# Optimization experiments

Measured on AMD Instinct MI355X. Metric: run time of the kernel, lower is better.

## Reference

```python
import jax, jax.numpy as jnp
import numpy as np

L = 4       # num_layers
H = 64      # hidden
EPS_BN = 1e-5


def _edge_mlp_bn(e, W1, b1, W2, b2, g, bt):
    # Sequential(Linear, ReLU, Linear, ReLU, BatchNorm1d) in training mode
    h = jax.nn.relu(e @ W1 + b1)
    h = jax.nn.relu(h @ W2 + b2)
    mu = jnp.mean(h, axis=0)
    var = jnp.mean((h - mu) ** 2, axis=0)  # biased variance (torch BN train)
    return (h - mu) * jax.lax.rsqrt(var + EPS_BN) * g + bt


def _bip_layer(src, tgt, ei, eattr, p, i):
    # p = (eW1, eb1, eW2, eb2, g, bt, lW, lb, rW), each stacked over layers
    eW1, eb1, eW2, eb2, g, bt, lW, lb, rW = (q[i] for q in p)
    emb = _edge_mlp_bn(eattr, eW1, eb1, eW2, eb2, g, bt)
    msg = jax.nn.relu(src[ei[0]] + emb)                         # [E, H]
    n_t = tgt.shape[0]
    agg = jax.ops.segment_sum(msg, ei[1], num_segments=n_t)
    cnt = jax.ops.segment_sum(jnp.ones((ei.shape[1],), msg.dtype), ei[1],
                              num_segments=n_t)
    out = agg / jnp.maximum(cnt, 1.0)[:, None]                  # mean aggr
    out = out @ lW + lb + tgt @ rW                              # lin_l + lin_r
    nrm = jnp.linalg.norm(out, axis=-1, keepdims=True)
    return out / jnp.maximum(nrm, 1e-12)                        # F.normalize


def setup_inputs() -> dict:
    key = jax.random.key(0)
    ks = iter(jax.random.split(key, 64))
    Nv = Nc = 100000
    Ev = Ec = 1250000
    d = {}
    d["var_node_features"] = jax.random.normal(next(ks), (Nv, 2), jnp.float32)
    d["con_node_features"] = jax.random.normal(next(ks), (Nc, 2), jnp.float32)
    d["edge_features_var"] = jax.random.normal(next(ks), (Ev, 1), jnp.float32)
    d["edge_features_con"] = jax.random.normal(next(ks), (Ec, 1), jnp.float32)
    d["edge_index_var"] = jax.random.randint(next(ks), (2, Ev), 0, Nv, jnp.int32)
    d["edge_index_con"] = jax.random.randint(next(ks), (2, Ec), 0, Nc, jnp.int32)

    def lin(k, shape, fan_in):
        return jax.random.normal(k, shape, jnp.float32) * (2.0 / fan_in) ** 0.5

    # node encoders: Linear(2,H), ReLU, Linear(H,H)
    for nm in ("enc_v", "enc_c"):
        d[nm + "_W1"] = lin(next(ks), (2, H), 2)
        d[nm + "_b1"] = jnp.zeros((H,), jnp.float32)
        d[nm + "_W2"] = lin(next(ks), (H, H), H)
        d[nm + "_b2"] = jnp.zeros((H,), jnp.float32)

    # bipartite layers (lv_* = layers_var, lc_* = layers_con), stacked over L
    for nm in ("lv", "lc"):
        d[nm + "_eW1"] = lin(next(ks), (L, 1, H), 1)
        d[nm + "_eb1"] = jnp.zeros((L, H), jnp.float32)
        d[nm + "_eW2"] = lin(next(ks), (L, H, H), H)
        d[nm + "_eb2"] = jnp.zeros((L, H), jnp.float32)
        d[nm + "_g"] = jnp.ones((L, H), jnp.float32)
        d[nm + "_bt"] = jnp.zeros((L, H), jnp.float32)
        d[nm + "_lW"] = lin(next(ks), (L, H, H), H)
        d[nm + "_lb"] = jnp.zeros((L, H), jnp.float32)
        d[nm + "_rW"] = lin(next(ks), (L, H, H), H)

    d["lin1_W"] = lin(next(ks), ((L + 1) * H, H), (L + 1) * H)
    d["lin1_b"] = jnp.zeros((H,), jnp.float32)
    d["lin2_W"] = lin(next(ks), (H, H), H)
    d["lin2_b"] = jnp.zeros((H,), jnp.float32)
    d["lin3_W"] = lin(next(ks), (H, H), H)
    d["lin3_b"] = jnp.zeros((H,), jnp.float32)
    d["lin4_W"] = lin(next(ks), (H, 2), H)
    d["lin4_b"] = jnp.zeros((2,), jnp.float32)
    return d


def reference(var_node_features, con_node_features, edge_features_var,
              edge_features_con, edge_index_var, edge_index_con,
              enc_v_W1, enc_v_b1, enc_v_W2, enc_v_b2,
              enc_c_W1, enc_c_b1, enc_c_W2, enc_c_b2,
              lv_eW1, lv_eb1, lv_eW2, lv_eb2, lv_g, lv_bt, lv_lW, lv_lb, lv_rW,
              lc_eW1, lc_eb1, lc_eW2, lc_eb2, lc_g, lc_bt, lc_lW, lc_lb, lc_rW,
              lin1_W, lin1_b, lin2_W, lin2_b, lin3_W, lin3_b, lin4_W, lin4_b):
    xv = jax.nn.relu(var_node_features @ enc_v_W1 + enc_v_b1) @ enc_v_W2 + enc_v_b2
    xc = jax.nn.relu(con_node_features @ enc_c_W1 + enc_c_b1) @ enc_c_W2 + enc_c_b2
    lvp = (lv_eW1, lv_eb1, lv_eW2, lv_eb2, lv_g, lv_bt, lv_lW, lv_lb, lv_rW)
    lcp = (lc_eW1, lc_eb1, lc_eW2, lc_eb2, lc_g, lc_bt, lc_lW, lc_lb, lc_rW)
    x_var = [xv]
    for i in range(L):
        # var -> con pass (layers_var), then con -> var pass (layers_con)
        xc = jax.nn.relu(_bip_layer(xv, xc, edge_index_var, edge_features_var, lvp, i))
        xv = jax.nn.relu(_bip_layer(xc, xv, edge_index_con, edge_features_con, lcp, i))
        x_var.append(xv)
    x = jnp.concatenate(x_var, axis=-1)                         # [Nv, (L+1)H]
    x = jax.nn.relu(x @ lin1_W + lin1_b)
    x = jax.nn.relu(x @ lin2_W + lin2_b)
    x = jax.nn.relu(x @ lin3_W + lin3_b)
    x = x @ lin4_W + lin4_b
    return jax.nn.log_softmax(x, axis=-1)
```

## Files before the change

### kernel.cpp

```cpp
#include <hip/hip_runtime.h>
#include <math.h>

__device__ __forceinline__ float readlane_f(float v, int l) {
    return __int_as_float(__builtin_amdgcn_readlane(__float_as_int(v), l));
}
__device__ __forceinline__ unsigned readlane_u(unsigned v, int l) {
    return (unsigned)__builtin_amdgcn_readlane((int)v, l);
}

__global__ __launch_bounds__(256) void enc_kernel(
    const float* __restrict__ feat, const float* __restrict__ W1,
    const float* __restrict__ b1, const float* __restrict__ W2,
    const float* __restrict__ b2, float* __restrict__ out, int N)
{
    __shared__ float sW2[64 * 64];
    __shared__ float sh1[64 * 64];
    const int n0 = blockIdx.x * 64;
    const int t = threadIdx.x;
    for (int idx = t; idx < 4096; idx += 256) sW2[idx] = W2[idx];
    for (int idx = t; idx < 4096; idx += 256) {
        int n = idx >> 6, j = idx & 63;
        int gn = n0 + n;
        float v = 0.f;
        if (gn < N) {
            float f0 = feat[gn * 2 + 0], f1 = feat[gn * 2 + 1];
            v = fmaxf(fmaf(f0, W1[j], fmaf(f1, W1[64 + j], b1[j])), 0.f);
        }
        sh1[idx] = v;
    }
    __syncthreads();
    for (int idx = t; idx < 4096; idx += 256) {
        int n = idx >> 6, k = idx & 63;
        int gn = n0 + n;
        if (gn >= N) continue;
        float acc = b2[k];
        const float* hrow = &sh1[n * 64];
        #pragma unroll 8
        for (int j = 0; j < 64; ++j) acc = fmaf(hrow[j], sW2[j * 64 + k], acc);
        out[gn * 64 + k] = acc;
    }
}

__global__ __launch_bounds__(256) void build_tables_all_kernel(
    const float* __restrict__ lv_eW1, const float* __restrict__ lv_eb1,
    const float* __restrict__ lv_eW2, const float* __restrict__ lv_eb2,
    const float* __restrict__ lc_eW1, const float* __restrict__ lc_eb1,
    const float* __restrict__ lc_eW2, const float* __restrict__ lc_eb2,
    float* __restrict__ PQ8, float* __restrict__ sortedT8)
{
    const int cfg = blockIdx.x;
    const int li = (cfg < 4) ? cfg : cfg - 4;
    const float* eW1 = ((cfg < 4) ? lv_eW1 : lc_eW1) + li * 64;
    const float* eb1 = ((cfg < 4) ? lv_eb1 : lc_eb1) + li * 64;
    const float* eW2 = ((cfg < 4) ? lv_eW2 : lc_eW2) + li * 4096;
    const float* eb2 = ((cfg < 4) ? lv_eb2 : lc_eb2) + li * 64;
    float* PQ = PQ8 + cfg * 65 * 128;
    float* sortedT = sortedT8 + cfg * 64;

    __shared__ float sa[64], sb[64], sT[64];
    __shared__ int srank[64];
    const int t = threadIdx.x;
    if (t < 64) {
        float a = eW1[t], b = eb1[t];
        sa[t] = a; sb[t] = b;
        sT[t] = (a != 0.f) ? (-b / a) : INFINITY;
    }
    __syncthreads();
    if (t < 64) {
        float Tj = sT[t];
        int r = 0;
        for (int i = 0; i < 64; ++i) {
            float Ti = sT[i];
            r += (Ti < Tj || (Ti == Tj && i < t)) ? 1 : 0;
        }
        srank[t] = r;
        sortedT[r] = Tj;
    }
    __syncthreads();
    for (int idx = t; idx < 65 * 64; idx += 256) {
        int iv = idx >> 6, k = idx & 63;
        float accP = 0.f, accQ = 0.f;
        for (int j = 0; j < 64; ++j) {
            float a = sa[j];
            bool act = (a > 0.f) ? (srank[j] < iv)
                                 : ((a < 0.f) ? (srank[j] >= iv) : (sb[j] > 0.f));
            if (act) {
                float w = eW2[j * 64 + k];
                accP = fmaf(a, w, accP);
                accQ = fmaf(sb[j], w, accQ);
            }
        }
        PQ[idx * 2 + 0] = accP;
        PQ[idx * 2 + 1] = accQ + eb2[k];
    }
}

__device__ __forceinline__ int interval_of(const float* sT, float ev)
{
    int iv = 0;
    #pragma unroll
    for (int s = 32; s >= 1; s >>= 1)
        if (iv + s <= 64 && sT[iv + s - 1] < ev) iv += s;
    return iv;
}

__global__ __launch_bounds__(256) void edge_stats_all_kernel(
    const float* __restrict__ efv, const float* __restrict__ efc, int Ev, int Ec,
    const float* __restrict__ PQ8, const float* __restrict__ sortedT8,
    double* __restrict__ stage, int NSB)
{
    const int cfg = blockIdx.y;
    const float* ef = (cfg < 4) ? efv : efc;
    const int E = (cfg < 4) ? Ev : Ec;
    const float2* __restrict__ PQg = (const float2*)(PQ8 + cfg * 65 * 128);
    const float* sortedT = sortedT8 + cfg * 64;

    __shared__ float sT[64];
    __shared__ double sred[2][4][64];
    const int t = threadIdx.x;
    if (t < 64) sT[t] = sortedT[t];
    __syncthreads();
    const int lane = t & 63, wave = t >> 6;
    const int gw = blockIdx.x * 4 + wave;
    const int nW = NSB * 4;
    double sum = 0.0, sq = 0.0;
    const int nTiles = (E + 63) >> 6;
    for (int tile = gw; tile < nTiles; tile += nW) {
        const int p = tile << 6;
        const int m = min(64, E - p);
        float ev = 0.f; int iv = 0;
        if (lane < m) {
            ev = ef[p + lane];
            iv = interval_of(sT, ev);
        }
        for (int c = 0; c < m; c += 16) {
            if (c + 16 <= m) {
                float h[16];
                #pragma unroll
                for (int k = 0; k < 16; ++k) {
                    float sev = readlane_f(ev, c + k);
                    int siv = __builtin_amdgcn_readlane(iv, c + k);
                    float2 pq = PQg[siv * 64 + lane];
                    h[k] = fmaxf(fmaf(sev, pq.x, pq.y), 0.f);
                }
                #pragma unroll
                for (int k = 0; k < 16; ++k) {
                    sum += (double)h[k];
                    sq = fma((double)h[k], (double)h[k], sq);
                }
            } else {
                for (int k = c; k < m; ++k) {
                    float sev = readlane_f(ev, k);
                    int siv = __builtin_amdgcn_readlane(iv, k);
                    float2 pq = PQg[siv * 64 + lane];
                    float h = fmaxf(fmaf(sev, pq.x, pq.y), 0.f);
                    sum += (double)h;
                    sq = fma((double)h, (double)h, sq);
                }
            }
        }
    }
    sred[0][wave][lane] = sum;
    sred[1][wave][lane] = sq;
    __syncthreads();
    if (t < 128) {
        int s = t >> 6, k = t & 63;
        double v = sred[s][0][k] + sred[s][1][k] + sred[s][2][k] + sred[s][3][k];
        stage[((size_t)(cfg * NSB + blockIdx.x) * 2 + s) * 64 + k] = v;
    }
}

__global__ __launch_bounds__(128) void bn_finalize_all_kernel(
    const double* __restrict__ stage, int NSB,
    const float* __restrict__ lv_g, const float* __restrict__ lv_bt,
    const float* __restrict__ lc_g, const float* __restrict__ lc_bt,
    int Ev, int Ec, float* __restrict__ stv)
{
    const int cfg = blockIdx.x;
    const int t = threadIdx.x;
    const int s = t >> 6, k = t & 63;
    double a = 0.0;
    for (int b = 0; b < NSB; ++b)
        a += stage[((size_t)(cfg * NSB + b) * 2 + s) * 64 + k];
    __shared__ double sh[2][64];
    sh[s][k] = a;
    __syncthreads();
    if (t < 64) {
        double En = (double)((cfg < 4) ? Ev : Ec);
        double mu = sh[0][k] / En;
        double var = sh[1][k] / En - mu * mu;
        if (var < 0.0) var = 0.0;
        const int li = (cfg < 4) ? cfg : cfg - 4;
        const float* g  = ((cfg < 4) ? lv_g  : lc_g)  + li * 64;
        const float* bt = ((cfg < 4) ? lv_bt : lc_bt) + li * 64;
        double sc = (double)g[k] / sqrt(var + 1e-5);
        stv[cfg * 128 + k] = (float)sc;
        stv[cfg * 128 + 64 + k] = (float)((double)bt[k] - mu * sc);
    }
}

__global__ void count_kernel(const int* __restrict__ tgt_idx,
                             int* __restrict__ cnt, int E)
{
    int i = blockIdx.x * blockDim.x + threadIdx.x;
    if (i < E) atomicAdd(&cnt[tgt_idx[i]], 1);
}

__global__ __launch_bounds__(256) void scan1_kernel(const int* __restrict__ cnt,
                                                    int* __restrict__ bsum, int N)
{
    __shared__ int sred[256];
    const int b = blockIdx.x, t = threadIdx.x;
    const int base = b * 1024;
    int s = 0;
    for (int i = t; i < 1024; i += 256) {
        int g = base + i;
        s += (g < N) ? cnt[g] : 0;
    }
    sred[t] = s; __syncthreads();
    for (int o = 128; o > 0; o >>= 1) {
        if (t < o) sred[t] += sred[t + o];
        __syncthreads();
    }
    if (t == 0) bsum[b] = sred[0];
}

__global__ __launch_bounds__(1024) void scan2_kernel(int* __restrict__ bsum, int G,
                                                     int* __restrict__ rowptr_last, int E)
{
    __shared__ int s[1024];
    const int t = threadIdx.x;
    int v = (t < G) ? bsum[t] : 0;
    s[t] = v; __syncthreads();
    for (int o = 1; o < 1024; o <<= 1) {
        int x = (t >= o) ? s[t - o] : 0;
        __syncthreads();
        s[t] += x;
        __syncthreads();
    }
    if (t < G) bsum[t] = s[t] - v;
    if (t == 0) *rowptr_last = E;
}

__global__ __launch_bounds__(256) void scan3_kernel(const int* __restrict__ cnt,
                                                    const int* __restrict__ bsum,
                                                    int* __restrict__ rowptr,
                                                    int* __restrict__ cursor, int N)
{
    __shared__ int sthr[256];
    const int b = blockIdx.x, t = threadIdx.x;
    const int base = b * 1024 + t * 4;
    int loc[4]; int run = 0;
    #pragma unroll
    for (int j = 0; j < 4; ++j) {
        int g = base + j;
        int c = (g < N) ? cnt[g] : 0;
        loc[j] = run; run += c;
    }
    sthr[t] = run; __syncthreads();
    int own = run;
    for (int o = 1; o < 256; o <<= 1) {
        int x = (t >= o) ? sthr[t - o] : 0;
        __syncthreads();
        sthr[t] += x;
        __syncthreads();
    }
    int ex = sthr[t] - own + bsum[b];
    #pragma unroll
    for (int j = 0; j < 4; ++j) {
        int g = base + j;
        if (g < N) { rowptr[g] = ex + loc[j]; cursor[g] = ex + loc[j]; }
    }
}

__global__ void scatter_kernel(const float* __restrict__ ef, const int* __restrict__ ei,
                               int* __restrict__ cursor, float* __restrict__ efp,
                               int* __restrict__ srcp, int E)
{
    int e = blockIdx.x * blockDim.x + threadIdx.x;
    if (e < E) {
        int tg = ei[E + e];
        int pos = atomicAdd(&cursor[tg], 1);
        efp[pos] = ef[e];
        srcp[pos] = ei[e];
    }
}

template <bool FUSE_ACC>
__global__ __launch_bounds__(256) void layer_kernel(
    const float* __restrict__ efp, const int* __restrict__ srcp,
    const int* __restrict__ rowptr, const float* __restrict__ src,
    float* __restrict__ tgt,
    const float* __restrict__ PQ, const float* __restrict__ sortedT,
    const float* __restrict__ st,
    const float* __restrict__ lW, const float* __restrict__ lb,
    const float* __restrict__ rW,
    const float* __restrict__ accW, float* __restrict__ acc, int N)
{
    __shared__ float sU[4096];
    __shared__ float sAgg[64][65];
    __shared__ float sT[64];
    __shared__ int   sRp[65];
    __shared__ float part[4][64];
    __shared__ float srn[64];

    const int t = threadIdx.x, lane = t & 63, wave = t >> 6;
    const int n0 = blockIdx.x * 64;
    const float2* __restrict__ PQg = (const float2*)PQ;

    for (int i = t; i < 64 * 65; i += 256) (&sAgg[0][0])[i] = 0.f;
    if (t < 64) sT[t] = sortedT[t];
    if (t < 65) sRp[t] = rowptr[min(n0 + t, N)];
    __syncthreads();

    const float ssv = st[lane], ttv = st[64 + lane];
    const int e0 = sRp[0], e1 = sRp[64];
    float racc = 0.f;
    for (int tb = e0 + wave * 64; tb < e1; tb += 256) {
        const int m = min(64, e1 - tb);
        float ev = 0.f; unsigned pk = 0; bool bndb = false;
        if (lane < m) {
            int g = tb + lane;
            ev = efp[g];
            unsigned is = (unsigned)srcp[g];
            int lo = 0;
            #pragma unroll
            for (int s = 32; s >= 1; s >>= 1) {
                int c = lo + s;
                if (c <= 63 && sRp[c] <= g) lo = c;
            }
            bndb = (g + 1 == sRp[lo + 1]);
            unsigned iv = (unsigned)interval_of(sT, ev);
            pk = is | (iv << 18) | ((unsigned)lo << 25) | (bndb ? (1u << 31) : 0u);
        }
        const unsigned long long bm = __ballot(bndb);
        for (int c = 0; c < m; c += 16) {
            if (c + 16 <= m) {
                float msg[16];
                #pragma unroll
                for (int k = 0; k < 16; ++k) {
                    float sev = readlane_f(ev, c + k);
                    unsigned spk = readlane_u(pk, c + k);
                    float2 pq = PQg[((spk >> 18) & 0x7Fu) * 64 + lane];
                    float h = fmaxf(fmaf(sev, pq.x, pq.y), 0.f);
                    msg[k] = fmaxf(src[(size_t)(spk & 0x3FFFFu) * 64 + lane]
                                   + fmaf(h, ssv, ttv), 0.f);
                }
                #pragma unroll
                for (int k = 0; k < 16; ++k) {
                    racc += msg[k];
                    if ((bm >> (c + k)) & 1ull) {
                        unsigned spk = readlane_u(pk, c + k);
                        int l = (int)((spk >> 25) & 63u);
                        float inv = 1.f / (float)(sRp[l + 1] - sRp[l]);
                        atomicAdd(&sAgg[l][lane], racc * inv);
                        racc = 0.f;
                    }
                }
            } else {
                for (int k = c; k < m; ++k) {
                    float sev = readlane_f(ev, k);
                    unsigned spk = readlane_u(pk, k);
                    float2 pq = PQg[((spk >> 18) & 0x7Fu) * 64 + lane];
                    float h = fmaxf(fmaf(sev, pq.x, pq.y), 0.f);
                    float msg = fmaxf(src[(size_t)(spk & 0x3FFFFu) * 64 + lane]
                                      + fmaf(h, ssv, ttv), 0.f);
                    racc += msg;
                    if ((bm >> k) & 1ull) {
                        int l = (int)((spk >> 25) & 63u);
                        float inv = 1.f / (float)(sRp[l + 1] - sRp[l]);
                        atomicAdd(&sAgg[l][lane], racc * inv);
                        racc = 0.f;
                    }
                }
            }
        }
        if (racc != 0.f) {
            unsigned spk = readlane_u(pk, m - 1);
            int l = (int)((spk >> 25) & 63u);
            float inv = 1.f / (float)(sRp[l + 1] - sRp[l]);
            atomicAdd(&sAgg[l][lane], racc * inv);
            racc = 0.f;
        }
    }
    __syncthreads();

    for (int idx = t; idx < 4096; idx += 256) sU[idx] = lW[idx];
    __syncthreads();
    const int n = lane;
    float o[16];
    {
        const float* mr = sAgg[n];
        for (int m4 = 0; m4 < 4; ++m4) {
            const int kb = (wave + m4 * 4) * 4;
            float o0 = 0, o1 = 0, o2 = 0, o3 = 0;
            #pragma unroll 8
            for (int j = 0; j < 64; ++j) {
                float mv = mr[j];
                float4 w4 = *reinterpret_cast<const float4*>(&sU[j * 64 + kb]);
                o0 = fmaf(mv, w4.x, o0); o1 = fmaf(mv, w4.y, o1);
                o2 = fmaf(mv, w4.z, o2); o3 = fmaf(mv, w4.w, o3);
            }
            o[m4 * 4 + 0] = o0; o[m4 * 4 + 1] = o1;
            o[m4 * 4 + 2] = o2; o[m4 * 4 + 3] = o3;
        }
    }
    __syncthreads();
    for (int idx = t; idx < 4096; idx += 256) sU[idx] = rW[idx];
    for (int idx = t; idx < 4096; idx += 256) {
        int nn = idx >> 6, j = idx & 63;
        int gn = n0 + nn;
        sAgg[nn][j] = (gn < N) ? tgt[(size_t)gn * 64 + j] : 0.f;
    }
    __syncthreads();
    float ssq = 0.f;
    {
        const float* tr = sAgg[n];
        for (int m4 = 0; m4 < 4; ++m4) {
            const int kb = (wave + m4 * 4) * 4;
            float o0 = o[m4 * 4 + 0], o1 = o[m4 * 4 + 1];
            float o2 = o[m4 * 4 + 2], o3 = o[m4 * 4 + 3];
            #pragma unroll 8
            for (int j = 0; j < 64; ++j) {
                float tv = tr[j];
                float4 w4 = *reinterpret_cast<const float4*>(&sU[j * 64 + kb]);
                o0 = fmaf(tv, w4.x, o0); o1 = fmaf(tv, w4.y, o1);
                o2 = fmaf(tv, w4.z, o2); o3 = fmaf(tv, w4.w, o3);
            }
            o0 += lb[kb + 0]; o1 += lb[kb + 1]; o2 += lb[kb + 2]; o3 += lb[kb + 3];
            o[m4 * 4 + 0] = o0; o[m4 * 4 + 1] = o1;
            o[m4 * 4 + 2] = o2; o[m4 * 4 + 3] = o3;
            ssq = fmaf(o0, o0, fmaf(o1, o1, fmaf(o2, o2, fmaf(o3, o3, ssq))));
        }
    }
    part[wave][n] = ssq;
    __syncthreads();
    if (t < 64) {
        float s = part[0][t] + part[1][t] + part[2][t] + part[3][t];
        srn[t] = 1.f / fmaxf(sqrtf(s), 1e-12f);
    }
    for (int m4 = 0; m4 < 4; ++m4) {
        const int kb = (wave + m4 * 4) * 4;
        sAgg[n][kb + 0] = o[m4 * 4 + 0];
        sAgg[n][kb + 1] = o[m4 * 4 + 1];
        sAgg[n][kb + 2] = o[m4 * 4 + 2];
        sAgg[n][kb + 3] = o[m4 * 4 + 3];
    }
    __syncthreads();
    for (int idx = t; idx < 4096; idx += 256) {
        int nn = idx >> 6, k = idx & 63;
        int gn = n0 + nn;
        float v = fmaxf((&sAgg[0][0])[nn * 65 + k] * srn[nn], 0.f);
        if (gn < N) tgt[(size_t)gn * 64 + k] = v;
        if (FUSE_ACC) (&sAgg[0][0])[nn * 65 + k] = v;
    }
    if (FUSE_ACC) {
        __syncthreads();
        for (int idx = t; idx < 4096; idx += 256) sU[idx] = accW[idx];
        __syncthreads();
        const float* xr = sAgg[n];
        const int gn = n0 + n;
        for (int m4 = 0; m4 < 4; ++m4) {
            const int kb = (wave + m4 * 4) * 4;
            float o0 = 0, o1 = 0, o2 = 0, o3 = 0;
            #pragma unroll 8
            for (int j = 0; j < 64; ++j) {
                float xv = xr[j];
                float4 w4 = *reinterpret_cast<const float4*>(&sU[j * 64 + kb]);
                o0 = fmaf(xv, w4.x, o0); o1 = fmaf(xv, w4.y, o1);
                o2 = fmaf(xv, w4.z, o2); o3 = fmaf(xv, w4.w, o3);
            }
            if (gn < N) {
                float4* ap = reinterpret_cast<float4*>(&acc[(size_t)gn * 64 + kb]);
                float4 old = *ap;
                *ap = make_float4(old.x + o0, old.y + o1, old.z + o2, old.w + o3);
            }
        }
    }
}

__global__ __launch_bounds__(256) void acc_gemm_init_kernel(
    const float* __restrict__ X, const float* __restrict__ W,
    float* __restrict__ acc, int N)
{
    __shared__ float sW[64 * 64];
    __shared__ float sX[64][65];
    const int n0 = blockIdx.x * 64;
    const int t = threadIdx.x;
    for (int idx = t; idx < 4096; idx += 256) sW[idx] = W[idx];
    for (int idx = t; idx < 4096; idx += 256) {
        int n = idx >> 6, j = idx & 63;
        int gn = n0 + n;
        sX[n][j] = (gn < N) ? X[gn * 64 + j] : 0.f;
    }
    __syncthreads();
    const int n = t & 63;
    const int gn = n0 + n;
    for (int m4 = 0; m4 < 4; ++m4) {
        int kb = ((t >> 6) + m4 * 4) * 4;
        float o0 = 0, o1 = 0, o2 = 0, o3 = 0;
        const float* xr = sX[n];
        #pragma unroll 8
        for (int j = 0; j < 64; ++j) {
            float xv = xr[j];
            float4 w4 = *reinterpret_cast<const float4*>(&sW[j * 64 + kb]);
            o0 = fmaf(xv, w4.x, o0); o1 = fmaf(xv, w4.y, o1);
            o2 = fmaf(xv, w4.z, o2); o3 = fmaf(xv, w4.w, o3);
        }
        if (gn < N)
            *reinterpret_cast<float4*>(&acc[(size_t)gn * 64 + kb]) =
                make_float4(o0, o1, o2, o3);
    }
}

__global__ __launch_bounds__(256) void final_kernel(
    const float* __restrict__ acc, const float* __restrict__ b1,
    const float* __restrict__ W2, const float* __restrict__ b2,
    const float* __restrict__ W3, const float* __restrict__ b3,
    const float* __restrict__ W4, const float* __restrict__ b4,
    float* __restrict__ out, int N)
{
    __shared__ float sW[64 * 64];
    __shared__ float sA[64][65], sB[64][65];
    __shared__ float sy[64][2];
    const int n0 = blockIdx.x * 64;
    const int t = threadIdx.x;
    for (int idx = t; idx < 4096; idx += 256) sW[idx] = W2[idx];
    for (int idx = t; idx < 4096; idx += 256) {
        int n = idx >> 6, j = idx & 63;
        int gn = n0 + n;
        sA[n][j] = (gn < N) ? fmaxf(acc[gn * 64 + j] + b1[j], 0.f) : 0.f;
    }
    __syncthreads();
    const int n = t & 63;
    for (int m4 = 0; m4 < 4; ++m4) {
        int kb = ((t >> 6) + m4 * 4) * 4;
        float o0 = 0, o1 = 0, o2 = 0, o3 = 0;
        const float* xr = sA[n];
        #pragma unroll 8
        for (int j = 0; j < 64; ++j) {
            float xv = xr[j];
            float4 w4 = *reinterpret_cast<const float4*>(&sW[j * 64 + kb]);
            o0 = fmaf(xv, w4.x, o0); o1 = fmaf(xv, w4.y, o1);
            o2 = fmaf(xv, w4.z, o2); o3 = fmaf(xv, w4.w, o3);
        }
        sB[n][kb + 0] = fmaxf(o0 + b2[kb + 0], 0.f);
        sB[n][kb + 1] = fmaxf(o1 + b2[kb + 1], 0.f);
        sB[n][kb + 2] = fmaxf(o2 + b2[kb + 2], 0.f);
        sB[n][kb + 3] = fmaxf(o3 + b2[kb + 3], 0.f);
    }
    __syncthreads();
    for (int idx = t; idx < 4096; idx += 256) sW[idx] = W3[idx];
    __syncthreads();
    for (int m4 = 0; m4 < 4; ++m4) {
        int kb = ((t >> 6) + m4 * 4) * 4;
        float o0 = 0, o1 = 0, o2 = 0, o3 = 0;
        const float* xr = sB[n];
        #pragma unroll 8
        for (int j = 0; j < 64; ++j) {
            float xv = xr[j];
            float4 w4 = *reinterpret_cast<const float4*>(&sW[j * 64 + kb]);
            o0 = fmaf(xv, w4.x, o0); o1 = fmaf(xv, w4.y, o1);
            o2 = fmaf(xv, w4.z, o2); o3 = fmaf(xv, w4.w, o3);
        }
        sA[n][kb + 0] = fmaxf(o0 + b3[kb + 0], 0.f);
        sA[n][kb + 1] = fmaxf(o1 + b3[kb + 1], 0.f);
        sA[n][kb + 2] = fmaxf(o2 + b3[kb + 2], 0.f);
        sA[n][kb + 3] = fmaxf(o3 + b3[kb + 3], 0.f);
    }
    __syncthreads();
    if (t < 128) {
        int nn = t >> 1, c = t & 1;
        float a = b4[c];
        for (int j = 0; j < 64; ++j) a = fmaf(sA[nn][j], W4[j * 2 + c], a);
        sy[nn][c] = a;
    }
    __syncthreads();
    if (t < 64) {
        int gn = n0 + t;
        if (gn < N) {
            float y0 = sy[t][0], y1 = sy[t][1];
            float m = fmaxf(y0, y1);
            float lse = m + logf(expf(y0 - m) + expf(y1 - m));
            out[gn * 2 + 0] = y0 - lse;
            out[gn * 2 + 1] = y1 - lse;
        }
    }
}

extern "C" void kernel_launch(void* const* d_in, const int* in_sizes, int n_in,
                              void* d_out, int out_size, void* d_ws, size_t ws_size,
                              hipStream_t stream)
{
    const float* varf    = (const float*)d_in[0];
    const float* conf    = (const float*)d_in[1];
    const float* ev_feat = (const float*)d_in[2];
    const float* ec_feat = (const float*)d_in[3];
    const int*   ei_var  = (const int*)d_in[4];
    const int*   ei_con  = (const int*)d_in[5];
    const float* enc_v_W1 = (const float*)d_in[6];
    const float* enc_v_b1 = (const float*)d_in[7];
    const float* enc_v_W2 = (const float*)d_in[8];
    const float* enc_v_b2 = (const float*)d_in[9];
    const float* enc_c_W1 = (const float*)d_in[10];
    const float* enc_c_b1 = (const float*)d_in[11];
    const float* enc_c_W2 = (const float*)d_in[12];
    const float* enc_c_b2 = (const float*)d_in[13];
    const float* lv_eW1 = (const float*)d_in[14];
    const float* lv_eb1 = (const float*)d_in[15];
    const float* lv_eW2 = (const float*)d_in[16];
    const float* lv_eb2 = (const float*)d_in[17];
    const float* lv_g   = (const float*)d_in[18];
    const float* lv_bt  = (const float*)d_in[19];
    const float* lv_lW  = (const float*)d_in[20];
    const float* lv_lb  = (const float*)d_in[21];
    const float* lv_rW  = (const float*)d_in[22];
    const float* lc_eW1 = (const float*)d_in[23];
    const float* lc_eb1 = (const float*)d_in[24];
    const float* lc_eW2 = (const float*)d_in[25];
    const float* lc_eb2 = (const float*)d_in[26];
    const float* lc_g   = (const float*)d_in[27];
    const float* lc_bt  = (const float*)d_in[28];
    const float* lc_lW  = (const float*)d_in[29];
    const float* lc_lb  = (const float*)d_in[30];
    const float* lc_rW  = (const float*)d_in[31];
    const float* lin1_W = (const float*)d_in[32];
    const float* lin1_b = (const float*)d_in[33];
    const float* lin2_W = (const float*)d_in[34];
    const float* lin2_b = (const float*)d_in[35];
    const float* lin3_W = (const float*)d_in[36];
    const float* lin3_b = (const float*)d_in[37];
    const float* lin4_W = (const float*)d_in[38];
    const float* lin4_b = (const float*)d_in[39];

    const int Nv = in_sizes[0] / 2, Nc = in_sizes[1] / 2;
    const int Ev = in_sizes[2], Ec = in_sizes[3];
    const int maxN = (Nv > Nc) ? Nv : Nc;
    const int NSB = 128;

    size_t need = (size_t)(8 * NSB * 2 * 64) * 8;
    need += ((size_t)Nv * 64 * 2 + (size_t)Nc * 64) * 4;
    need += (size_t)(8 * 65 * 128 + 8 * 64 + 8 * 128) * 4;
    need += ((size_t)Ev * 2 + (size_t)Ec * 2) * 4;
    need += ((size_t)Nc + 1 + (size_t)Nv + 1) * 4;
    need += ((size_t)maxN * 2 + 1024) * 4;
    if (ws_size < need) {
        hipMemsetAsync(d_out, 0, (size_t)out_size * sizeof(float), stream);
        return;
    }

    double* stage = (double*)d_ws;
    float* ws = (float*)(stage + (size_t)8 * NSB * 2 * 64);
    float* xv  = ws;  ws += (size_t)Nv * 64;
    float* xc  = ws;  ws += (size_t)Nc * 64;
    float* acc = ws;  ws += (size_t)Nv * 64;
    float* PQ8 = ws;      ws += 8 * 65 * 128;
    float* sortedT8 = ws; ws += 8 * 64;
    float* stv = ws;      ws += 8 * 128;
    float* efp_v = ws;            ws += Ev;
    int*   srcp_v = (int*)ws;     ws += Ev;
    float* efp_c = ws;            ws += Ec;
    int*   srcp_c = (int*)ws;     ws += Ec;
    int*   rowptr_v = (int*)ws;   ws += Nc + 1;
    int*   rowptr_c = (int*)ws;   ws += Nv + 1;
    int*   cnt    = (int*)ws;     ws += maxN;
    int*   cursor = (int*)ws;     ws += maxN;
    int*   bsum   = (int*)ws;     ws += 1024;

    const dim3 blk(256);
    const int gbV = (Nv + 63) / 64, gbC = (Nc + 63) / 64;

    enc_kernel<<<gbV, blk, 0, stream>>>(varf, enc_v_W1, enc_v_b1, enc_v_W2, enc_v_b2, xv, Nv);
    enc_kernel<<<gbC, blk, 0, stream>>>(conf, enc_c_W1, enc_c_b1, enc_c_W2, enc_c_b2, xc, Nc);

    {
        hipMemsetAsync(cnt, 0, (size_t)Nc * sizeof(int), stream);
        count_kernel<<<(Ev + 255) / 256, blk, 0, stream>>>(ei_var + Ev, cnt, Ev);
        int G = (Nc + 1023) / 1024;
        scan1_kernel<<<G, blk, 0, stream>>>(cnt, bsum, Nc);
        scan2_kernel<<<1, 1024, 0, stream>>>(bsum, G, rowptr_v + Nc, Ev);
        scan3_kernel<<<G, blk, 0, stream>>>(cnt, bsum, rowptr_v, cursor, Nc);
        scatter_kernel<<<(Ev + 255) / 256, blk, 0, stream>>>(ev_feat, ei_var, cursor,
                                                             efp_v, srcp_v, Ev);
        hipMemsetAsync(cnt, 0, (size_t)Nv * sizeof(int), stream);
        count_kernel<<<(Ec + 255) / 256, blk, 0, stream>>>(ei_con + Ec, cnt, Ec);
        G = (Nv + 1023) / 1024;
        scan1_kernel<<<G, blk, 0, stream>>>(cnt, bsum, Nv);
        scan2_kernel<<<1, 1024, 0, stream>>>(bsum, G, rowptr_c + Nv, Ec);
        scan3_kernel<<<G, blk, 0, stream>>>(cnt, bsum, rowptr_c, cursor, Nv);
        scatter_kernel<<<(Ec + 255) / 256, blk, 0, stream>>>(ec_feat, ei_con, cursor,
                                                             efp_c, srcp_c, Ec);
    }

    build_tables_all_kernel<<<8, blk, 0, stream>>>(
        lv_eW1, lv_eb1, lv_eW2, lv_eb2, lc_eW1, lc_eb1, lc_eW2, lc_eb2, PQ8, sortedT8);
    edge_stats_all_kernel<<<dim3(NSB, 8), blk, 0, stream>>>(
        ev_feat, ec_feat, Ev, Ec, PQ8, sortedT8, stage, NSB);
    bn_finalize_all_kernel<<<8, 128, 0, stream>>>(
        stage, NSB, lv_g, lv_bt, lc_g, lc_bt, Ev, Ec, stv);

    acc_gemm_init_kernel<<<gbV, blk, 0, stream>>>(xv, lin1_W, acc, Nv);

    for (int i = 0; i < 4; ++i) {
        layer_kernel<false><<<gbC, blk, 0, stream>>>(
            efp_v, srcp_v, rowptr_v, xv, xc,
            PQ8 + i * 65 * 128, sortedT8 + i * 64, stv + i * 128,
            lv_lW + i * 4096, lv_lb + i * 64, lv_rW + i * 4096,
            nullptr, nullptr, Nc);
        layer_kernel<true><<<gbV, blk, 0, stream>>>(
            efp_c, srcp_c, rowptr_c, xc, xv,
            PQ8 + (4 + i) * 65 * 128, sortedT8 + (4 + i) * 64, stv + (4 + i) * 128,
            lc_lW + i * 4096, lc_lb + i * 64, lc_rW + i * 4096,
            lin1_W + (i + 1) * 4096, acc, Nv);
    }

    final_kernel<<<gbV, blk, 0, stream>>>(acc, lin1_b, lin2_W, lin2_b,
                                          lin3_W, lin3_b, lin4_W, lin4_b,
                                          (float*)d_out, Nv);
}
```

Baseline: 2.146 ms.

## Drop LDS weight staging, use wave-uniform scalar weight loads, float partial sums

```diff
diff --git a/kernel.cpp b/kernel.cpp
--- a/kernel.cpp
+++ b/kernel.cpp
@@ -143,20 +143,26 @@
                     float2 pq = PQg[siv * 64 + lane];
                     h[k] = fmaxf(fmaf(sev, pq.x, pq.y), 0.f);
                 }
+                float s16 = 0.f, q16 = 0.f;
                 #pragma unroll
                 for (int k = 0; k < 16; ++k) {
-                    sum += (double)h[k];
-                    sq = fma((double)h[k], (double)h[k], sq);
+                    s16 += h[k];
+                    q16 = fmaf(h[k], h[k], q16);
                 }
+                sum += (double)s16;
+                sq  += (double)q16;
             } else {
+                float s16 = 0.f, q16 = 0.f;
                 for (int k = c; k < m; ++k) {
                     float sev = readlane_f(ev, k);
                     int siv = __builtin_amdgcn_readlane(iv, k);
                     float2 pq = PQg[siv * 64 + lane];
                     float h = fmaxf(fmaf(sev, pq.x, pq.y), 0.f);
-                    sum += (double)h;
-                    sq = fma((double)h, (double)h, sq);
+                    s16 += h;
+                    q16 = fmaf(h, h, q16);
                 }
+                sum += (double)s16;
+                sq  += (double)q16;
             }
         }
     }
@@ -287,7 +293,7 @@
 }
 
 template <bool FUSE_ACC>
-__global__ __launch_bounds__(256) void layer_kernel(
+__global__ __launch_bounds__(256, 6) void layer_kernel(
     const float* __restrict__ efp, const int* __restrict__ srcp,
     const int* __restrict__ rowptr, const float* __restrict__ src,
     float* __restrict__ tgt,
@@ -297,7 +303,6 @@
     const float* __restrict__ rW,
     const float* __restrict__ accW, float* __restrict__ acc, int N)
 {
-    __shared__ float sU[4096];
     __shared__ float sAgg[64][65];
     __shared__ float sT[64];
     __shared__ int   sRp[65];
@@ -385,19 +390,19 @@
     }
     __syncthreads();
 
-    for (int idx = t; idx < 4096; idx += 256) sU[idx] = lW[idx];
-    __syncthreads();
+    const float4* __restrict__ lW4 = (const float4*)lW;
+    const float4* __restrict__ rW4 = (const float4*)rW;
     const int n = lane;
     float o[16];
     {
         const float* mr = sAgg[n];
         for (int m4 = 0; m4 < 4; ++m4) {
-            const int kb = (wave + m4 * 4) * 4;
+            const int kq = __builtin_amdgcn_readfirstlane(wave + m4 * 4);
             float o0 = 0, o1 = 0, o2 = 0, o3 = 0;
             #pragma unroll 8
             for (int j = 0; j < 64; ++j) {
                 float mv = mr[j];
-                float4 w4 = *reinterpret_cast<const float4*>(&sU[j * 64 + kb]);
+                float4 w4 = lW4[j * 16 + kq];
                 o0 = fmaf(mv, w4.x, o0); o1 = fmaf(mv, w4.y, o1);
                 o2 = fmaf(mv, w4.z, o2); o3 = fmaf(mv, w4.w, o3);
             }
@@ -406,7 +411,6 @@
         }
     }
     __syncthreads();
-    for (int idx = t; idx < 4096; idx += 256) sU[idx] = rW[idx];
     for (int idx = t; idx < 4096; idx += 256) {
         int nn = idx >> 6, j = idx & 63;
         int gn = n0 + nn;
@@ -417,13 +421,14 @@
     {
         const float* tr = sAgg[n];
         for (int m4 = 0; m4 < 4; ++m4) {
-            const int kb = (wave + m4 * 4) * 4;
+            const int kq = __builtin_amdgcn_readfirstlane(wave + m4 * 4);
+            const int kb = kq * 4;
             float o0 = o[m4 * 4 + 0], o1 = o[m4 * 4 + 1];
             float o2 = o[m4 * 4 + 2], o3 = o[m4 * 4 + 3];
             #pragma unroll 8
             for (int j = 0; j < 64; ++j) {
                 float tv = tr[j];
-                float4 w4 = *reinterpret_cast<const float4*>(&sU[j * 64 + kb]);
+                float4 w4 = rW4[j * 16 + kq];
                 o0 = fmaf(tv, w4.x, o0); o1 = fmaf(tv, w4.y, o1);
                 o2 = fmaf(tv, w4.z, o2); o3 = fmaf(tv, w4.w, o3);
             }
@@ -456,17 +461,17 @@
     }
     if (FUSE_ACC) {
         __syncthreads();
-        for (int idx = t; idx < 4096; idx += 256) sU[idx] = accW[idx];
-        __syncthreads();
+        const float4* __restrict__ aW4 = (const float4*)accW;
         const float* xr = sAgg[n];
         const int gn = n0 + n;
         for (int m4 = 0; m4 < 4; ++m4) {
-            const int kb = (wave + m4 * 4) * 4;
+            const int kq = __builtin_amdgcn_readfirstlane(wave + m4 * 4);
+            const int kb = kq * 4;
             float o0 = 0, o1 = 0, o2 = 0, o3 = 0;
             #pragma unroll 8
             for (int j = 0; j < 64; ++j) {
                 float xv = xr[j];
-                float4 w4 = *reinterpret_cast<const float4*>(&sU[j * 64 + kb]);
+                float4 w4 = aW4[j * 16 + kq];
                 o0 = fmaf(xv, w4.x, o0); o1 = fmaf(xv, w4.y, o1);
                 o2 = fmaf(xv, w4.z, o2); o3 = fmaf(xv, w4.w, o3);
             }
@@ -636,7 +641,7 @@
     const int Nv = in_sizes[0] / 2, Nc = in_sizes[1] / 2;
     const int Ev = in_sizes[2], Ec = in_sizes[3];
     const int maxN = (Nv > Nc) ? Nv : Nc;
-    const int NSB = 128;
+    const int NSB = 256;
 
     size_t need = (size_t)(8 * NSB * 2 * 64) * 8;
     need += ((size_t)Nv * 64 * 2 + (size_t)Nc * 64) * 4;
```

Result: slower. 2.217 ms (+3.3%).
